# Kernel tuning notes

Hardware: AMD Instinct MI355X
Metric: run time of the kernel (lower is better)

## Reference

```python
import jax, jax.numpy as jnp
import numpy as np

LAYERS, BLOCKS = 10, 4
RES_CH, DIL_CH, SKIP_CH, CLASSES = 32, 32, 512, 256
K = 2                      # kernel_size
OUTPUT_LENGTH = 4096
N_LAYERS = LAYERS * BLOCKS
DILATIONS = [2 ** i for _ in range(BLOCKS) for i in range(LAYERS)]
BATCH, SEQ = 8, 8192       # SEQ divisible by max dilation 512; SEQ - 4092 >= OUTPUT_LENGTH


def conv1d(x, w, dilation=1):
    # x: (N, C_in, L), w: (C_out, C_in, K); causal valid dilated conv
    return jax.lax.conv_general_dilated(
        x, w, window_strides=(1,), padding='VALID',
        rhs_dilation=(dilation,), dimension_numbers=('NCH', 'OIH', 'NCH'))


def setup_inputs() -> dict:
    key = jax.random.key(0)
    ks = jax.random.split(key, 8)
    s = 0.1
    return {
        'x': jax.random.normal(ks[0], (BATCH, 1, SEQ), jnp.float32),
        'start_w': jax.random.normal(ks[1], (RES_CH, 1, 1), jnp.float32) * s,
        'filter_w': jax.random.normal(ks[2], (N_LAYERS, DIL_CH, RES_CH, K), jnp.float32) * s,
        'gate_w': jax.random.normal(ks[3], (N_LAYERS, DIL_CH, RES_CH, K), jnp.float32) * s,
        'res_w': jax.random.normal(ks[4], (N_LAYERS, RES_CH, DIL_CH, 1), jnp.float32) * s,
        'skip_w': jax.random.normal(ks[5], (N_LAYERS, SKIP_CH, DIL_CH, 1), jnp.float32) * s,
        'end_w': jax.random.normal(ks[6], (CLASSES, SKIP_CH, 1), jnp.float32) * s,
        'end_b': jax.random.normal(ks[7], (CLASSES,), jnp.float32) * s,
    }


def reference(x, start_w, filter_w, gate_w, res_w, skip_w, end_w, end_b):
    h = conv1d(x, start_w)                       # (N, RES_CH, SEQ)
    skip = None
    for i in range(N_LAYERS):
        d = DILATIONS[i]
        f = jnp.tanh(conv1d(h, filter_w[i], d))   # (N, DIL_CH, L - d*(K-1))
        g = jax.nn.sigmoid(conv1d(h, gate_w[i], d))
        z = f * g
        s = conv1d(z, skip_w[i])                  # (N, SKIP_CH, L')
        skip = s if skip is None else skip[:, :, -s.shape[2]:] + s
        h = conv1d(z, res_w[i]) + h[:, :, d * (K - 1):]
    out = conv1d(jax.nn.relu(skip), end_w) + end_b[None, :, None]
    out = out[:, :, -OUTPUT_LENGTH:]              # (N, CLASSES, OUTPUT_LENGTH)
    n, c, l = out.shape
    return out.transpose(0, 2, 1).reshape(n * l, c)
```

## Files before the change

kernel.cpp:

```cpp
#include <hip/hip_runtime.h>
#include <hip/hip_bf16.h>


#define BATCH   8
#define SEQ     8192
#define RES_CH  32
#define DIL_CH  32
#define SKIP_CH 512
#define CLASSES 256
#define NLAYERS 40
#define OUTLEN  4096
#define PSTART  (SEQ - OUTLEN)
#define QTOT    (NLAYERS * DIL_CH)

typedef __attribute__((ext_vector_type(8))) short bf16x8;
typedef __attribute__((ext_vector_type(4))) short short4_t;
typedef __attribute__((ext_vector_type(4))) float f32x4;

__device__ __forceinline__ float fast_sigmoid(float x) {
    return __builtin_amdgcn_rcpf(1.0f + __expf(-x));
}
__device__ __forceinline__ float fast_tanh(float x) {
    return 1.0f - 2.0f * __builtin_amdgcn_rcpf(1.0f + __expf(2.0f * x));
}
__device__ __forceinline__ short f2bf(float x) {
    unsigned u = __float_as_uint(x);
    unsigned r = (u + 0x7fffu + ((u >> 16) & 1u)) >> 16;
    return (short)r;
}
__device__ __forceinline__ float bf2f(short s) {
    return __uint_as_float(((unsigned)(unsigned short)s) << 16);
}
__device__ __forceinline__ int tswz(int row, int cb) {
    return row * 64 + (cb ^ (((row & 3) << 4) | ((row & 4) << 3)));
}

#define GLOAD_LDS16(g, l)                                                    \
    __builtin_amdgcn_global_load_lds(                                        \
        (const __attribute__((address_space(1))) unsigned int*)(g),          \
        (__attribute__((address_space(3))) unsigned int*)(l), 16, 0, 0)

__global__ __launch_bounds__(256) void k_prep(
    const float* __restrict__ x, const float* __restrict__ sw,
    const float* __restrict__ fw, const float* __restrict__ gw,
    const float* __restrict__ rw, const float* __restrict__ wsk,
    const float* __restrict__ ew,
    float* __restrict__ hf, short* __restrict__ hb,
    short* __restrict__ wA, short* __restrict__ wR,
    short* __restrict__ wskB, short* __restrict__ ewB)
{
    const int gt = blockIdx.x * 256 + threadIdx.x;
    const int gn = gridDim.x * 256;
    for (int idx = gt; idx < BATCH * SEQ; idx += gn) {
        float v = x[idx];
        float* hp = hf + (size_t)idx * RES_CH;
        short* bp = hb + (size_t)idx * RES_CH;
#pragma unroll
        for (int c = 0; c < RES_CH; ++c) {
            float t = v * sw[c];
            hp[c] = t;
            bp[c] = f2bf(t);
        }
    }
    for (int idx = gt; idx < NLAYERS * 64 * 64; idx += gn) {
        int k = idx & 63, rho = (idx >> 6) & 63, i = idx >> 12;
        int tap = k >> 5, c = k & 31;
        int fgsel = rho >> 5, rr = rho & 31;
        int fp = rr >> 4, gg = (rr >> 2) & 3, e = rr & 3;
        int o = gg * 8 + fp * 4 + e;
        float v = fgsel ? gw[((i * 32 + o) * 32 + c) * 2 + tap]
                        : fw[((i * 32 + o) * 32 + c) * 2 + tap];
        wA[idx] = f2bf(v);
    }
    for (int idx = gt; idx < NLAYERS * 1024; idx += gn)
        wR[idx] = f2bf(rw[idx]);
    for (int idx = gt; idx < SKIP_CH * QTOT; idx += gn) {
        int s = idx / QTOT, q = idx - s * QTOT;
        int i = q >> 5, o = q & 31;
        wskB[idx] = f2bf(wsk[((size_t)i * SKIP_CH + s) * 32 + o]);
    }
    for (int idx = gt; idx < CLASSES * SKIP_CH; idx += gn)
        ewB[idx] = f2bf(ew[idx]);
}

template<bool OWNED>
__device__ __forceinline__ void chunk_body(
    int cp0, bool bglob, bool last, int d, int tog,
    const short* __restrict__ hbb, const float* __restrict__ hfb,
    float* __restrict__ hfo, short* __restrict__ hbo,
    short* __restrict__ zbb, int liq,
    const char* trd, char* tw,
    const bf16x8 (&av)[4][2], const bf16x8 (&avr)[2],
    f32x4 (*carryc)[2][2],
    int r, int g14)
{
    int pl[2]; bool pv[2];
#pragma unroll
    for (int fj = 0; fj < 2; ++fj) {
        int p = cp0 + fj * 16 + r;
        pv[fj] = p < SEQ;
        pl[fj] = pv[fj] ? p : SEQ - 1;
    }

    bf16x8 bv[2][2];
    if (bglob) {
#pragma unroll
        for (int fj = 0; fj < 2; ++fj) {
            bv[fj][0] = *(const bf16x8*)(hbb + (pl[fj] - d) * 32 + g14 * 8);
            bv[fj][1] = *(const bf16x8*)(hbb + pl[fj] * 32 + g14 * 8);
        }
    } else {
#pragma unroll
        for (int fj = 0; fj < 2; ++fj) {
            int tr = pl[fj] - tog;
            bv[fj][0] = *(const bf16x8*)(trd + tswz(tr - d, g14 * 16));
            bv[fj][1] = *(const bf16x8*)(trd + tswz(tr, g14 * 16));
        }
    }

    const f32x4 zero4 = {0.f, 0.f, 0.f, 0.f};
    f32x4 acc[4][2];
#pragma unroll
    for (int fi = 0; fi < 4; ++fi)
#pragma unroll
        for (int fj = 0; fj < 2; ++fj) acc[fi][fj] = zero4;
#pragma unroll
    for (int kt = 0; kt < 2; ++kt)
#pragma unroll
        for (int fi = 0; fi < 4; ++fi)
#pragma unroll
            for (int fj = 0; fj < 2; ++fj)
                acc[fi][fj] = __builtin_amdgcn_mfma_f32_16x16x32_bf16(
                    av[fi][kt], bv[fj][kt], acc[fi][fj], 0, 0, 0);

    bf16x8 zv8[2];
#pragma unroll
    for (int fj = 0; fj < 2; ++fj)
#pragma unroll
        for (int fp = 0; fp < 2; ++fp)
#pragma unroll
            for (int e = 0; e < 4; ++e)
                zv8[fj][fp * 4 + e] =
                    f2bf(fast_tanh(acc[fp][fj][e]) *
                         fast_sigmoid(acc[fp + 2][fj][e]));

    if constexpr (OWNED) {
#pragma unroll
        for (int fj = 0; fj < 2; ++fj)
            if (pv[fj] && pl[fj] >= PSTART) {
                short* zp = zbb + (size_t)(pl[fj] - PSTART) * QTOT + liq;
                *(bf16x8*)(zp + g14 * 8) = zv8[fj];
            }
    }

    f32x4 racc[2][2];
    if constexpr (OWNED) {
        if (bglob) {
#pragma unroll
            for (int fi = 0; fi < 2; ++fi)
#pragma unroll
                for (int fj = 0; fj < 2; ++fj)
                    racc[fi][fj] = *(const f32x4*)(hfb + pl[fj] * 32 + fi * 16 + g14 * 4);
        } else {
#pragma unroll
            for (int fi = 0; fi < 2; ++fi)
#pragma unroll
                for (int fj = 0; fj < 2; ++fj)
                    racc[fi][fj] = (*carryc)[fi][fj];
        }
    } else {
#pragma unroll
        for (int fj = 0; fj < 2; ++fj)
#pragma unroll
            for (int fi = 0; fi < 2; ++fi) {
                short4_t hv;
                if (bglob)
                    hv = *(const short4_t*)(hbb + pl[fj] * 32 + fi * 16 + g14 * 4);
                else
                    hv = *(const short4_t*)(trd + tswz(pl[fj] - tog, fi * 32 + g14 * 8));
                f32x4 cv;
#pragma unroll
                for (int e = 0; e < 4; ++e) cv[e] = bf2f(hv[e]);
                racc[fi][fj] = cv;
            }
    }

#pragma unroll
    for (int fi = 0; fi < 2; ++fi)
#pragma unroll
        for (int fj = 0; fj < 2; ++fj)
            racc[fi][fj] = __builtin_amdgcn_mfma_f32_16x16x32_bf16(
                avr[fi], zv8[fj], racc[fi][fj], 0, 0, 0);

    if constexpr (OWNED) {
#pragma unroll
        for (int fi = 0; fi < 2; ++fi)
#pragma unroll
            for (int fj = 0; fj < 2; ++fj)
                (*carryc)[fi][fj] = racc[fi][fj];
    }

    if (!last) {
#pragma unroll
        for (int fj = 0; fj < 2; ++fj)
            if (pv[fj]) {
                int tr = pl[fj] - tog;
#pragma unroll
                for (int fi = 0; fi < 2; ++fi) {
                    short4_t sv;
#pragma unroll
                    for (int e = 0; e < 4; ++e) sv[e] = f2bf(racc[fi][fj][e]);
                    *(short4_t*)(tw + tswz(tr, fi * 32 + g14 * 8)) = sv;
                }
            }
    } else {
        if constexpr (OWNED) {
#pragma unroll
            for (int fj = 0; fj < 2; ++fj)
                if (pv[fj]) {
#pragma unroll
                    for (int fi = 0; fi < 2; ++fi) {
                        *(f32x4*)(hfo + pl[fj] * 32 + fi * 16 + g14 * 4) = racc[fi][fj];
                        short4_t sv;
#pragma unroll
                        for (int e = 0; e < 4; ++e) sv[e] = f2bf(racc[fi][fj][e]);
                        *(short4_t*)(hbo + pl[fj] * 32 + fi * 16 + g14 * 4) = sv;
                    }
                }
        }
    }
}

template<int LC, int S, int TH, int NTB>
__global__ __launch_bounds__(256, 2) void k_fused(
    const float* __restrict__ hfin, const short* __restrict__ hbin,
    float* __restrict__ hfout, short* __restrict__ hbout,
    const short* __restrict__ wAg, const short* __restrict__ wRg,
    short* __restrict__ Z, int li0, int pminIn, int hsum, int segbase)
{
    constexpr int TROWS = TH + S;
    constexpr int OPW = S / 128;
    __shared__ short tile[NTB][TROWS][32];

    const int lane = threadIdx.x & 63;
    const int w    = threadIdx.x >> 6;
    const int r = lane & 15, g14 = lane >> 4;
    const int b = blockIdx.y;
    const int seg0 = segbase + blockIdx.x * S;
    const int tog  = seg0 - TH;

    const float* hfb = hfin + (size_t)b * SEQ * RES_CH;
    const short* hbb = hbin + (size_t)b * SEQ * RES_CH;
    float* hfo = hfout + (size_t)b * SEQ * RES_CH;
    short* hbo = hbout + (size_t)b * SEQ * RES_CH;
    short* zbb = Z + (size_t)b * OUTLEN * QTOT;

    f32x4 carry[OPW][2][2];
    int Ht = hsum, pmt = pminIn;

#pragma unroll 1
    for (int t = 0; t < LC; ++t) {
        const int d = 1 << ((li0 + t) % 10);
        Ht -= d; pmt += d;
        const bool bglob = (t == 0);
        const bool last  = (t == LC - 1);
        const short* wAl = wAg + (li0 + t) * 4096;
        const short* wRl = wRg + (li0 + t) * 1024;
        const int liq = (li0 + t) * DIL_CH;
        char* tw = (char*)&tile[t & (NTB - 1)][0][0];
        const char* trd = (const char*)&tile[(t + NTB - 1) & (NTB - 1)][0][0];

        bf16x8 av[4][2];
#pragma unroll
        for (int fi = 0; fi < 4; ++fi)
#pragma unroll
            for (int kt = 0; kt < 2; ++kt)
                av[fi][kt] = *(const bf16x8*)(wAl + (fi * 16 + r) * 64 + kt * 32 + g14 * 8);
        bf16x8 avr[2];
#pragma unroll
        for (int fi = 0; fi < 2; ++fi)
            avr[fi] = *(const bf16x8*)(wRl + (fi * 16 + r) * 32 + g14 * 8);

#pragma unroll
        for (int oc = 0; oc < OPW; ++oc) {
            const int cp0 = seg0 + (oc * 4 + w) * 32;
            chunk_body<true>(cp0, bglob, last, d, tog, hbb, hfb, hfo, hbo,
                             zbb, liq, trd, tw, av, avr, &carry[oc], r, g14);
        }
        int lo = seg0 - Ht; if (lo < pmt) lo = pmt;
        const int nh = (seg0 - lo + 31) >> 5;
#pragma unroll 2
        for (int hc = w; hc < nh; hc += 4) {
            const int cp0 = seg0 - (hc + 1) * 32;
            chunk_body<false>(cp0, bglob, last, d, tog, hbb, hfb, hfo, hbo,
                              zbb, liq, trd, tw, av, avr, nullptr, r, g14);
        }
        __syncthreads();
    }
}

__global__ __launch_bounds__(256) void k_skip_m97(
    const short* __restrict__ Z, const short* __restrict__ wskB,
    short* __restrict__ skipb)
{
    __shared__ short At[2][128 * 32];
    __shared__ short Bt[2][128 * 32];

    const int bid = blockIdx.x;
    const int b    = bid & 7;
    const int rest = bid >> 3;
    const int sb   = rest & 3;
    const int pb   = rest >> 2;
    const int s0   = sb * 128;
    const int p0   = pb * 128;

    const int lane = threadIdx.x & 63;
    const int w    = threadIdx.x >> 6;
    const int r = lane & 15, g14 = lane >> 4;
    const int soff = (w >> 1) * 64;
    const int poff = (w & 1) * 64;

    const short* Ab = wskB + (size_t)s0 * QTOT;
    const short* Bb = Z + ((size_t)b * OUTLEN + p0) * QTOT;

    const int rb = w * 32;
    const int l4 = lane >> 2;
    const int c4 = lane & 3;
    const int csw = c4 ^ ((l4 >> 1) & 3);
    const int rsw = (g14 ^ ((r >> 1) & 3)) * 8;

#define SK_STAGE(bf, kt)                                                      \
    {                                                                         \
        _Pragma("unroll") for (int j = 0; j < 2; ++j) {                       \
            const short* ga = Ab + (size_t)(rb + j * 16 + l4) * QTOT          \
                                 + (kt) * 32 + csw * 8;                       \
            GLOAD_LDS16(ga, &At[bf][(rb + j * 16) * 32]);                     \
            const short* gb = Bb + (size_t)(rb + j * 16 + l4) * QTOT          \
                                 + (kt) * 32 + csw * 8;                       \
            GLOAD_LDS16(gb, &Bt[bf][(rb + j * 16) * 32]);                     \
        }                                                                     \
    }

    f32x4 acc[4][4];
    const f32x4 zero4 = {0.f, 0.f, 0.f, 0.f};
#pragma unroll
    for (int fi = 0; fi < 4; ++fi)
#pragma unroll
        for (int fj = 0; fj < 4; ++fj) acc[fi][fj] = zero4;

    SK_STAGE(0, 0)
    __syncthreads();

    int cur = 0;
#pragma unroll 1
    for (int kt = 0; kt < QTOT / 32; ++kt) {
        if (kt + 1 < QTOT / 32) SK_STAGE(cur ^ 1, kt + 1)

        bf16x8 av[4], bv[4];
#pragma unroll
        for (int fi = 0; fi < 4; ++fi)
            av[fi] = *(const bf16x8*)&At[cur][(soff + fi * 16 + r) * 32 + rsw];
#pragma unroll
        for (int fj = 0; fj < 4; ++fj)
            bv[fj] = *(const bf16x8*)&Bt[cur][(poff + fj * 16 + r) * 32 + rsw];

#pragma unroll
        for (int fi = 0; fi < 4; ++fi)
#pragma unroll
            for (int fj = 0; fj < 4; ++fj)
                acc[fi][fj] = __builtin_amdgcn_mfma_f32_16x16x32_bf16(
                    av[fi], bv[fj], acc[fi][fj], 0, 0, 0);

        __syncthreads();
        cur ^= 1;
    }

    short* skb = skipb + (size_t)b * OUTLEN * SKIP_CH;
#pragma unroll
    for (int fj = 0; fj < 4; ++fj) {
        int p = p0 + poff + fj * 16 + r;
#pragma unroll
        for (int fi = 0; fi < 4; ++fi) {
            int s = s0 + soff + fi * 16 + g14 * 4;
            short4_t v;
#pragma unroll
            for (int e = 0; e < 4; ++e) v[e] = f2bf(fmaxf(acc[fi][fj][e], 0.f));
            *(short4_t*)(skb + (size_t)p * SKIP_CH + s) = v;
        }
    }
}

__global__ __launch_bounds__(256) void k_end_m97(
    const short* __restrict__ skipB, const short* __restrict__ ewB,
    const float* __restrict__ eb, float* __restrict__ out)
{
    __shared__ short At[2][128 * 32];
    __shared__ short Bt[2][128 * 32];

    const int bid = blockIdx.x;
    const int b    = bid & 7;
    const int rest = bid >> 3;
    const int cb   = rest & 1;
    const int pb   = rest >> 1;
    const int c0   = cb * 128;
    const int p0   = pb * 128;

    const int lane = threadIdx.x & 63;
    const int w    = threadIdx.x >> 6;
    const int r = lane & 15, g14 = lane >> 4;
    const int soff = (w >> 1) * 64;
    const int poff = (w & 1) * 64;

    const short* Ab = ewB + (size_t)c0 * SKIP_CH;
    const short* Bb = skipB + ((size_t)b * OUTLEN + p0) * SKIP_CH;

    const int rb = w * 32;
    const int l4 = lane >> 2;
    const int c4 = lane & 3;
    const int csw = c4 ^ ((l4 >> 1) & 3);
    const int rsw = (g14 ^ ((r >> 1) & 3)) * 8;

#define EK_STAGE(bf, kt)                                                      \
    {                                                                         \
        _Pragma("unroll") for (int j = 0; j < 2; ++j) {                       \
            const short* ga = Ab + (size_t)(rb + j * 16 + l4) * SKIP_CH       \
                                 + (kt) * 32 + csw * 8;                       \
            GLOAD_LDS16(ga, &At[bf][(rb + j * 16) * 32]);                     \
            const short* gb = Bb + (size_t)(rb + j * 16 + l4) * SKIP_CH       \
                                 + (kt) * 32 + csw * 8;                       \
            GLOAD_LDS16(gb, &Bt[bf][(rb + j * 16) * 32]);                     \
        }                                                                     \
    }

    f32x4 acc[4][4];
    const f32x4 zero4 = {0.f, 0.f, 0.f, 0.f};
#pragma unroll
    for (int fi = 0; fi < 4; ++fi)
#pragma unroll
        for (int fj = 0; fj < 4; ++fj) acc[fi][fj] = zero4;

    EK_STAGE(0, 0)
    __syncthreads();

    int cur = 0;
#pragma unroll 1
    for (int kt = 0; kt < SKIP_CH / 32; ++kt) {
        if (kt + 1 < SKIP_CH / 32) EK_STAGE(cur ^ 1, kt + 1)

        bf16x8 av[4], bv[4];
#pragma unroll
        for (int fi = 0; fi < 4; ++fi)
            av[fi] = *(const bf16x8*)&At[cur][(soff + fi * 16 + r) * 32 + rsw];
#pragma unroll
        for (int fj = 0; fj < 4; ++fj)
            bv[fj] = *(const bf16x8*)&Bt[cur][(poff + fj * 16 + r) * 32 + rsw];

#pragma unroll
        for (int fi = 0; fi < 4; ++fi)
#pragma unroll
            for (int fj = 0; fj < 4; ++fj)
                acc[fi][fj] = __builtin_amdgcn_mfma_f32_16x16x32_bf16(
                    av[fi], bv[fj], acc[fi][fj], 0, 0, 0);

        __syncthreads();
        cur ^= 1;
    }

#pragma unroll
    for (int fj = 0; fj < 4; ++fj) {
        int p = p0 + poff + fj * 16 + r;
#pragma unroll
        for (int fi = 0; fi < 4; ++fi) {
            int cls = c0 + soff + fi * 16 + g14 * 4;
            f32x4 bias = *(const f32x4*)(eb + cls);
            f32x4 v;
#pragma unroll
            for (int e = 0; e < 4; ++e) v[e] = acc[fi][fj][e] + bias[e];
            *(f32x4*)(out + ((size_t)b * OUTLEN + p) * CLASSES + cls) = v;
        }
    }
}

extern "C" void kernel_launch(void* const* d_in, const int* in_sizes, int n_in,
                              void* d_out, int out_size, void* d_ws, size_t ws_size,
                              hipStream_t stream) {
    const float* x   = (const float*)d_in[0];
    const float* sw  = (const float*)d_in[1];
    const float* fw  = (const float*)d_in[2];
    const float* gw  = (const float*)d_in[3];
    const float* rw  = (const float*)d_in[4];
    const float* wsk = (const float*)d_in[5];
    const float* ew  = (const float*)d_in[6];
    const float* eb  = (const float*)d_in[7];
    float* out = (float*)d_out;

    const size_t HN = (size_t)BATCH * SEQ * RES_CH;
    float* hf0 = (float*)d_ws;
    float* hf1 = hf0 + HN;
    short* hb0 = (short*)(hf1 + HN);
    short* hb1 = hb0 + HN;
    short* Z     = hb1 + HN;
    short* skipb = Z + (size_t)BATCH * OUTLEN * QTOT;
    short* wA    = skipb + (size_t)BATCH * OUTLEN * SKIP_CH;
    short* wR    = wA + NLAYERS * 64 * 64;
    short* wskB  = wR + NLAYERS * 32 * 32;
    short* ewB   = wskB + (size_t)SKIP_CH * QTOT;

    k_prep<<<dim3(1024), 256, 0, stream>>>(x, sw, fw, gw, rw, wsk, ew,
                                           hf0, hb0, wA, wR, wskB, ewB);

    float* hf[2] = {hf0, hf1};
    short* hb[2] = {hb0, hb1};
    int cur = 0, pmin = 0;
    for (int dec = 0; dec < 4; ++dec) {
        int li0 = dec * 10;
        int segbase = pmin + 255;
        int nseg = (SEQ - segbase + 255) / 256;
        k_fused<8, 256, 288, 2><<<dim3(nseg, BATCH), 256, 0, stream>>>(
            hf[cur], hb[cur], hf[cur ^ 1], hb[cur ^ 1], wA, wR, Z,
            li0, pmin, 255, segbase);
        cur ^= 1; pmin = segbase;
        segbase = pmin + 768;
        nseg = (SEQ - segbase + 255) / 256;
        k_fused<2, 256, 512, 1><<<dim3(nseg, BATCH), 256, 0, stream>>>(
            hf[cur], hb[cur], hf[cur ^ 1], hb[cur ^ 1], wA, wR, Z,
            li0 + 8, pmin, 768, segbase);
        cur ^= 1; pmin = segbase;
    }

    k_skip_m97<<<dim3(1024), 256, 0, stream>>>(Z, wskB, skipb);
    k_end_m97<<<dim3(512), 256, 0, stream>>>(skipb, ewB, eb, out);
}
```

Baseline: 354.7 us.

## Use 8-wave blocks with smaller owned segments and fuse gated activation math

The fused WaveNet layer kernel now launches 512 threads (8 waves) per block and owns 128 positions per block instead of 256. Four waves each take one owned chunk, and the halo chunks are spread across all eight waves, which doubles the grid size. The tanh*sigmoid gate is merged into a single expression using one reciprocal, with clamped exponents. Shrinking the owned segment raises the ratio of halo recompute to owned work, and the larger blocks may increase register and LDS pressure.

```diff
diff --git a/kernel.cpp b/kernel.cpp
--- a/kernel.cpp
+++ b/kernel.cpp
@@ -17,12 +17,6 @@
 typedef __attribute__((ext_vector_type(4))) short short4_t;
 typedef __attribute__((ext_vector_type(4))) float f32x4;
 
-__device__ __forceinline__ float fast_sigmoid(float x) {
-    return __builtin_amdgcn_rcpf(1.0f + __expf(-x));
-}
-__device__ __forceinline__ float fast_tanh(float x) {
-    return 1.0f - 2.0f * __builtin_amdgcn_rcpf(1.0f + __expf(2.0f * x));
-}
 __device__ __forceinline__ short f2bf(float x) {
     unsigned u = __float_as_uint(x);
     unsigned r = (u + 0x7fffu + ((u >> 16) & 1u)) >> 16;
@@ -30,6 +24,11 @@
 }
 __device__ __forceinline__ float bf2f(short s) {
     return __uint_as_float(((unsigned)(unsigned short)s) << 16);
+}
+__device__ __forceinline__ float zact(float f, float g) {
+    float a = __expf(fminf(-2.0f * f, 80.0f));
+    float b = __expf(fminf(-g, 80.0f));
+    return (1.0f - a) * __builtin_amdgcn_rcpf((1.0f + a) * (1.0f + b));
 }
 __device__ __forceinline__ int tswz(int row, int cb) {
     return row * 64 + (cb ^ (((row & 3) << 4) | ((row & 4) << 3)));
@@ -141,8 +140,7 @@
 #pragma unroll
             for (int e = 0; e < 4; ++e)
                 zv8[fj][fp * 4 + e] =
-                    f2bf(fast_tanh(acc[fp][fj][e]) *
-                         fast_sigmoid(acc[fp + 2][fj][e]));
+                    f2bf(zact(acc[fp][fj][e], acc[fp + 2][fj][e]));
 
     if constexpr (OWNED) {
 #pragma unroll
@@ -232,14 +230,14 @@
 }
 
 template<int LC, int S, int TH, int NTB>
-__global__ __launch_bounds__(256, 2) void k_fused(
+__global__ __launch_bounds__(512, 2) void k_fused8(
     const float* __restrict__ hfin, const short* __restrict__ hbin,
     float* __restrict__ hfout, short* __restrict__ hbout,
     const short* __restrict__ wAg, const short* __restrict__ wRg,
     short* __restrict__ Z, int li0, int pminIn, int hsum, int segbase)
 {
     constexpr int TROWS = TH + S;
-    constexpr int OPW = S / 128;
+    constexpr int NOWN = S / 32;
     __shared__ short tile[NTB][TROWS][32];
 
     const int lane = threadIdx.x & 63;
@@ -255,7 +253,7 @@
     short* hbo = hbout + (size_t)b * SEQ * RES_CH;
     short* zbb = Z + (size_t)b * OUTLEN * QTOT;
 
-    f32x4 carry[OPW][2][2];
+    f32x4 carry[2][2];
     int Ht = hsum, pmt = pminIn;
 
 #pragma unroll 1
@@ -281,16 +279,15 @@
         for (int fi = 0; fi < 2; ++fi)
             avr[fi] = *(const bf16x8*)(wRl + (fi * 16 + r) * 32 + g14 * 8);
 
-#pragma unroll
-        for (int oc = 0; oc < OPW; ++oc) {
-            const int cp0 = seg0 + (oc * 4 + w) * 32;
+        if (w < NOWN) {
+            const int cp0 = seg0 + w * 32;
             chunk_body<true>(cp0, bglob, last, d, tog, hbb, hfb, hfo, hbo,
-                             zbb, liq, trd, tw, av, avr, &carry[oc], r, g14);
+                             zbb, liq, trd, tw, av, avr, &carry, r, g14);
         }
         int lo = seg0 - Ht; if (lo < pmt) lo = pmt;
         const int nh = (seg0 - lo + 31) >> 5;
 #pragma unroll 2
-        for (int hc = w; hc < nh; hc += 4) {
+        for (int hc = (w + NOWN) & 7; hc < nh; hc += 8) {
             const int cp0 = seg0 - (hc + 1) * 32;
             chunk_body<false>(cp0, bglob, last, d, tog, hbb, hfb, hfo, hbo,
                               zbb, liq, trd, tw, av, avr, nullptr, r, g14);
@@ -515,14 +512,14 @@
     for (int dec = 0; dec < 4; ++dec) {
         int li0 = dec * 10;
         int segbase = pmin + 255;
-        int nseg = (SEQ - segbase + 255) / 256;
-        k_fused<8, 256, 288, 2><<<dim3(nseg, BATCH), 256, 0, stream>>>(
+        int nseg = (SEQ - segbase + 127) / 128;
+        k_fused8<8, 128, 288, 2><<<dim3(nseg, BATCH), 512, 0, stream>>>(
             hf[cur], hb[cur], hf[cur ^ 1], hb[cur ^ 1], wA, wR, Z,
             li0, pmin, 255, segbase);
         cur ^= 1; pmin = segbase;
         segbase = pmin + 768;
-        nseg = (SEQ - segbase + 255) / 256;
-        k_fused<2, 256, 512, 1><<<dim3(nseg, BATCH), 256, 0, stream>>>(
+        nseg = (SEQ - segbase + 127) / 128;
+        k_fused8<2, 128, 512, 1><<<dim3(nseg, BATCH), 512, 0, stream>>>(
             hf[cur], hb[cur], hf[cur ^ 1], hb[cur ^ 1], wA, wR, Z,
             li0 + 8, pmin, 768, segbase);
         cur ^= 1; pmin = segbase;
```

After: 446.3 us. +25.8%, slower.
